# Performance work log

Hardware: AMD Instinct MI355X
Metric: run time of the kernel (lower is better)

Reference implementation:

```python
import jax, jax.numpy as jnp
import numpy as np

B, S = 8, 1024
DM = 512            # d_model arg
D = 2 * DM          # actual feature width (1024)
H = 16
DK = D // H         # 64
DV = 2 * 32         # per-head value dim (2*d_v) = 64
DI = 2048           # d_inner
K = 4               # d_conv, dilation 2 -> effective 7, pad 3 each side
EPS = 1e-6


def setup_inputs() -> dict:
    key = jax.random.key(0)
    ks = jax.random.split(key, 16)
    s = lambda k, shape, fan: jax.random.normal(k, shape, jnp.float32) / np.sqrt(fan)
    return {
        "x": jax.random.normal(ks[0], (B, S, D), jnp.float32),
        "mask": jnp.ones((B, 1, 1, S), jnp.int32),
        "gamma": jnp.ones((D,), jnp.float32),
        "wq": s(ks[1], (D, H * DK), D),
        "wk": s(ks[2], (D, H * DK), D),
        "wv": s(ks[3], (D, H * DV), D),
        "wo": s(ks[4], (H * DV, D), H * DV),
        "w1": s(ks[5], (DM, DI), DM),
        "b1": jnp.zeros((DI,), jnp.float32),
        "cw": s(ks[6], (DI, 1, K), K),   # depthwise conv kernel [O, I/groups=1, K]
        "cb": jnp.zeros((DI,), jnp.float32),
        "w2": s(ks[7], (DM, DI), DM),
        "b2": jnp.zeros((DI,), jnp.float32),
        "wp": s(ks[8], (DI, D), DI),
        "bp": jnp.zeros((D,), jnp.float32),
    }


def reference(x, mask, gamma, wq, wk, wv, wo, w1, b1, cw, cb, w2, b2, wp, bp):
    # RMSNorm
    nrm = x * jax.lax.rsqrt(jnp.mean(x * x, axis=-1, keepdims=True) + EPS) * gamma
    # Multi-head attention
    q = (nrm @ wq).reshape(B, S, H, DK).transpose(0, 2, 1, 3)
    k = (nrm @ wk).reshape(B, S, H, DK).transpose(0, 2, 1, 3)
    v = (nrm @ wv).reshape(B, S, H, DV).transpose(0, 2, 1, 3)
    scores = jnp.einsum('bhqd,bhkd->bhqk', q, k) / np.sqrt(DK).astype(np.float32)
    scores = jnp.where(mask == 0, jnp.float32(-1e9), scores)
    attn = jax.nn.softmax(scores, axis=-1)
    ctx = jnp.einsum('bhqk,bhkd->bhqd', attn, v)        # [B,H,S,DV]
    ctx = ctx.transpose(0, 2, 1, 3).reshape(B, S, H * DV)
    out = ctx @ wo                                       # [B,S,D]
    # split into two halves
    f_in, s_in = out[:, :, :D // 2], out[:, :, D // 2:]
    # FirstSection: linear -> depthwise dilated conv (padding 'same')
    f = f_in @ w1 + b1                                   # [B,S,DI]
    f = f.transpose(0, 2, 1)                             # [B,DI,S]
    f = jax.lax.conv_general_dilated(
        f, cw, window_strides=(1,), padding=[(3, 3)], rhs_dilation=(2,),
        feature_group_count=DI, dimension_numbers=('NCH', 'OIH', 'NCH'))
    f = (f + cb[None, :, None]).transpose(0, 2, 1)       # [B,S,DI]
    # SecondSection: linear + relu
    sec = jax.nn.relu(s_in @ w2 + b2)                    # [B,S,DI]
    gated = f * sec
    return x + (gated @ wp + bp)
```

## Files before the change

kernel.cpp:

```cpp
#include <hip/hip_runtime.h>

typedef unsigned short u16;
typedef __bf16 bf16x8 __attribute__((ext_vector_type(8)));
typedef short  s16x8  __attribute__((ext_vector_type(8)));
typedef float  f32x4  __attribute__((ext_vector_type(4)));

#define LDSPAD 72

#define GLOAD16(gp, lp) __builtin_amdgcn_global_load_lds( \
  (__attribute__((address_space(1))) unsigned int*)(unsigned long long)(const void*)(gp), \
  (__attribute__((address_space(3))) unsigned int*)(lp), 16, 0, 0)

static __device__ __forceinline__ u16 f2bf(float f){
  union { float f; unsigned int u; } v; v.f = f;
  unsigned int r = v.u + 0x7fffu + ((v.u >> 16) & 1u);
  return (u16)(r >> 16);
}
static __device__ __forceinline__ float bf2f(u16 u){
  union { unsigned int u; float f; } v; v.u = ((unsigned int)u) << 16; return v.f;
}
static __device__ __forceinline__ unsigned fbits(float f){
  union { float f; unsigned u; } v; v.f = f; return v.u;
}

__global__ __launch_bounds__(256) void wtrans4_kernel(
    const float* __restrict__ in0, const float* __restrict__ in1,
    const float* __restrict__ in2, const float* __restrict__ in3,
    u16* __restrict__ out0, u16* __restrict__ out1,
    u16* __restrict__ out2, u16* __restrict__ out3, int K, int N){
  __shared__ float tile[32][33];
  int z = blockIdx.z;
  const float* in = (z == 0) ? in0 : (z == 1) ? in1 : (z == 2) ? in2 : in3;
  u16* out = (z == 0) ? out0 : (z == 1) ? out1 : (z == 2) ? out2 : out3;
  int n0 = blockIdx.x * 32, k0 = blockIdx.y * 32;
  int tx = threadIdx.x, ty = threadIdx.y;
  #pragma unroll
  for (int i = 0; i < 4; ++i)
    tile[ty + i*8][tx] = in[(size_t)(k0 + ty + i*8) * N + n0 + tx];
  __syncthreads();
  #pragma unroll
  for (int i = 0; i < 4; ++i)
    out[(size_t)(n0 + ty + i*8) * K + k0 + tx] = f2bf(tile[tx][ty + i*8]);
}

__global__ __launch_bounds__(256) void cwtrans_kernel(const float* __restrict__ cw,
                                                      float* __restrict__ cwT){
  int i = blockIdx.x * 256 + threadIdx.x;
  int c = i >> 2, j = i & 3;
  cwT[j * 2048 + c] = cw[i];
}

__global__ __launch_bounds__(256) void rmsnorm_kernel(const float* __restrict__ x,
                                                      const float* __restrict__ gamma,
                                                      u16* __restrict__ out){
  int row = blockIdx.x;
  const float* xr = x + (size_t)row * 1024;
  int tid = threadIdx.x;
  float4 xv = *(const float4*)(xr + tid * 4);
  float ss = xv.x*xv.x + xv.y*xv.y + xv.z*xv.z + xv.w*xv.w;
  #pragma unroll
  for (int off = 1; off < 64; off <<= 1) ss += __shfl_xor(ss, off);
  __shared__ float wsum[4];
  if ((tid & 63) == 0) wsum[tid >> 6] = ss;
  __syncthreads();
  float tot = wsum[0] + wsum[1] + wsum[2] + wsum[3];
  float r = rsqrtf(tot * (1.0f/1024.0f) + 1e-6f);
  const float4 gv = *(const float4*)(gamma + tid * 4);
  u16* o = out + (size_t)row * 1024 + tid * 4;
  o[0] = f2bf(xv.x * r * gv.x);
  o[1] = f2bf(xv.y * r * gv.y);
  o[2] = f2bf(xv.z * r * gv.z);
  o[3] = f2bf(xv.w * r * gv.w);
}

template<int EPI>
__global__ __launch_bounds__(256) void gemm128_kernel(
    const u16* __restrict__ A, int lda,
    const u16* __restrict__ Bt,
    const float* __restrict__ bias,
    const float* __restrict__ resid,
    u16* __restrict__ outb, float* __restrict__ outf,
    u16* __restrict__ vt,
    int N, int K, float scale, int nm)
{
  __shared__ __align__(16) u16 As[2][128*64];
  __shared__ __align__(16) u16 Bs[2][128*64];
  int tid = threadIdx.x;
  int wid = tid >> 6, lane = tid & 63;
  int fr = lane & 15, fq = lane >> 4;
  int wr = wid >> 1, wc = wid & 1;
  int l = (int)blockIdx.x;
  int m0 = (l % nm) * 128, n0 = (l / nm) * 128;
  int srow = lane >> 3;
  int csw  = (lane & 7) ^ srow;
  int c7   = fr & 7;
  f32x4 acc[4][4] = {};

  const u16* Abase = A  + (size_t)m0 * lda;
  const u16* Bbase = Bt + (size_t)n0 * K;

  auto STAGE = [&](int bsel, int kt){
    int k0 = kt << 6;
    #pragma unroll
    for (int i = 0; i < 4; ++i){
      int r = i*32 + wid*8;
      GLOAD16(Abase + (size_t)(r + srow) * lda + k0 + csw*8, &As[bsel][r*64]);
      GLOAD16(Bbase + (size_t)(r + srow) * K   + k0 + csw*8, &Bs[bsel][r*64]);
    }
  };

  int nt = K >> 6;
  STAGE(0, 0);
  __syncthreads();
  for (int kt = 0; kt < nt; ++kt){
    int cur = kt & 1;
    if (kt + 1 < nt) STAGE(cur ^ 1, kt + 1);
    #pragma unroll
    for (int ks = 0; ks < 2; ++ks){
      bf16x8 av[4], bv[4];
      #pragma unroll
      for (int mi = 0; mi < 4; ++mi)
        av[mi] = *(const bf16x8*)&As[cur][(wr*64 + mi*16 + fr)*64 + (((ks*4 + fq) ^ c7) * 8)];
      #pragma unroll
      for (int ni = 0; ni < 4; ++ni)
        bv[ni] = *(const bf16x8*)&Bs[cur][(wc*64 + ni*16 + fr)*64 + (((ks*4 + fq) ^ c7) * 8)];
      #pragma unroll
      for (int mi = 0; mi < 4; ++mi)
        #pragma unroll
        for (int ni = 0; ni < 4; ++ni)
          acc[mi][ni] = __builtin_amdgcn_mfma_f32_16x16x32_bf16(av[mi], bv[ni], acc[mi][ni], 0, 0, 0);
    }
    __syncthreads();
  }

  if (EPI == 5 && n0 >= 2048){
    u16* Ct = &As[0][0];
    #pragma unroll
    for (int p = 0; p < 2; ++p){
      __syncthreads();
      if (wc == p){
        #pragma unroll
        for (int ni = 0; ni < 4; ++ni)
          #pragma unroll
          for (int mi = 0; mi < 4; ++mi){
            int cl = ni*16 + fr;
            int rl = wr*64 + mi*16 + fq*4;
            uint2 pk;
            pk.x = (unsigned)f2bf(acc[mi][ni][0]) | ((unsigned)f2bf(acc[mi][ni][1]) << 16);
            pk.y = (unsigned)f2bf(acc[mi][ni][2]) | ((unsigned)f2bf(acc[mi][ni][3]) << 16);
            *(uint2*)&Ct[cl*136 + rl] = pk;
          }
      }
      __syncthreads();
      #pragma unroll
      for (int ci = 0; ci < 4; ++ci){
        int qq = ci*256 + tid;
        int c = qq >> 4, off = (qq & 15) * 8;
        uint4 v = *(const uint4*)&Ct[c*136 + off];
        *(uint4*)&vt[(size_t)(n0 - 2048 + p*64 + c) * 8192 + m0 + off] = v;
      }
    }
    return;
  }

  #pragma unroll
  for (int ni = 0; ni < 4; ++ni){
    int col = n0 + wc*64 + ni*16 + fr;
    float bvv = (EPI >= 1 && EPI <= 3) ? bias[col] : 0.0f;
    float scl = (EPI == 5) ? ((col < 1024) ? scale : 1.0f) : scale;
    #pragma unroll
    for (int mi = 0; mi < 4; ++mi){
      #pragma unroll
      for (int j = 0; j < 4; ++j){
        int row = m0 + wr*64 + mi*16 + fq*4 + j;
        float vv = acc[mi][ni][j] * scl + bvv;
        if (EPI == 2) vv = fmaxf(vv, 0.0f);
        size_t idx = (size_t)row * N + col;
        if (EPI == 3) outf[idx] = vv + resid[idx];
        else          outb[idx] = f2bf(vv);
      }
    }
  }
}

__global__ __launch_bounds__(256) void attn_kernel(
    const u16* __restrict__ qkv, const u16* __restrict__ Vt,
    const int* __restrict__ mask, u16* __restrict__ ctx)
{
  __shared__ __align__(16) u16 Ks[64*64];
  __shared__ __align__(16) u16 Vs[64*64];
  __shared__ __align__(16) u16 Ps[64][LDSPAD];
  int tid = threadIdx.x;
  int wid = tid >> 6, lane = tid & 63;
  int fr = lane & 15, fq = lane >> 4;
  int i = (int)blockIdx.x;
  int wg = (i & 7) * 256 + (i >> 3);
  int bh = wg >> 4;
  int q0 = (wg & 15) * 64;
  int b = bh >> 4, h = bh & 15;

  const u16* qb  = qkv + (size_t)b * 1024 * 3072 + h * 64;
  const u16* kb  = qb + 1024;
  const u16* vtb = Vt + (size_t)(h * 64) * 8192 + b * 1024;

  int lrow = lane >> 3;
  int cs   = (lane & 7) ^ lrow;
  int wbase = wid * 16;
  int c7 = fr & 7;

  bf16x8 qf[2];
  {
    const u16* qp = qb + (size_t)(q0 + wid*16 + fr) * 3072 + fq * 8;
    qf[0] = *(const bf16x8*)(qp);
    qf[1] = *(const bf16x8*)(qp + 32);
  }
  f32x4 acc[4];
  #pragma unroll
  for (int k = 0; k < 4; ++k) acc[k] = (f32x4){0.f, 0.f, 0.f, 0.f};
  float mrun = -1e30f, lsum = 0.f;

  auto STAGE = [&](int t){
    int kv0 = t * 64;
    #pragma unroll
    for (int k = 0; k < 2; ++k){
      int r = wbase + k*8 + lrow;
      GLOAD16(kb  + (size_t)(kv0 + r) * 3072 + cs * 8, &Ks[(wbase + k*8) * 64]);
      GLOAD16(vtb + (size_t)r * 8192 + kv0 + cs * 8,   &Vs[(wbase + k*8) * 64]);
    }
  };

  STAGE(0);
  for (int t = 0; t < 16; ++t){
    int kv0 = t * 64;
    __syncthreads();
    bf16x8 kf[2][4], vf[2][4];
    #pragma unroll
    for (int ks = 0; ks < 2; ++ks)
      #pragma unroll
      for (int nt = 0; nt < 4; ++nt){
        kf[ks][nt] = *(const bf16x8*)&Ks[(nt*16 + fr)*64 + (((ks*4 + fq) ^ c7) * 8)];
        vf[ks][nt] = *(const bf16x8*)&Vs[(nt*16 + fr)*64 + (((ks*4 + fq) ^ c7) * 8)];
      }
    int mv1 = mask[b * 1024 + kv0 + lane];
    __syncthreads();
    if (t + 1 < 16) STAGE(t + 1);

    f32x4 sc[4];
    #pragma unroll
    for (int nt = 0; nt < 4; ++nt) sc[nt] = (f32x4){0.f, 0.f, 0.f, 0.f};
    __builtin_amdgcn_s_setprio(1);
    #pragma unroll
    for (int ks = 0; ks < 2; ++ks)
      #pragma unroll
      for (int nt = 0; nt < 4; ++nt)
        sc[nt] = __builtin_amdgcn_mfma_f32_16x16x32_bf16(kf[ks][nt], qf[ks], sc[nt], 0, 0, 0);
    __builtin_amdgcn_s_setprio(0);

    if (!__all(mv1 != 0)){
      #pragma unroll
      for (int nt = 0; nt < 4; ++nt){
        int4 mv = *(const int4*)&mask[b * 1024 + kv0 + nt*16 + fq*4];
        int mvals[4] = {mv.x, mv.y, mv.z, mv.w};
        #pragma unroll
        for (int j = 0; j < 4; ++j)
          sc[nt][j] = mvals[j] ? sc[nt][j] : -1e9f;
      }
    }

    float m01 = fmaxf(fmaxf(sc[0][0], sc[0][1]), fmaxf(sc[0][2], sc[0][3]));
    float m11 = fmaxf(fmaxf(sc[1][0], sc[1][1]), fmaxf(sc[1][2], sc[1][3]));
    float m21 = fmaxf(fmaxf(sc[2][0], sc[2][1]), fmaxf(sc[2][2], sc[2][3]));
    float m31 = fmaxf(fmaxf(sc[3][0], sc[3][1]), fmaxf(sc[3][2], sc[3][3]));
    float pmax = fmaxf(fmaxf(m01, m11), fmaxf(m21, m31));
    pmax = fmaxf(pmax, __shfl_xor(pmax, 16));
    pmax = fmaxf(pmax, __shfl_xor(pmax, 32));
    if (!__all(pmax <= mrun + 8.0f)){
      float mnew = fmaxf(mrun, pmax);
      float corr = exp2f(mrun - mnew);
      #pragma unroll
      for (int nt = 0; nt < 4; ++nt)
        #pragma unroll
        for (int j = 0; j < 4; ++j)
          acc[nt][j] *= corr;
      lsum *= corr;
      mrun = mnew;
    }
    float p[4][4];
    float ls = 0.f;
    #pragma unroll
    for (int nt = 0; nt < 4; ++nt)
      #pragma unroll
      for (int j = 0; j < 4; ++j){
        float pv = exp2f(sc[nt][j] - mrun);
        p[nt][j] = pv;
        ls += pv;
      }
    lsum += ls;

    #pragma unroll
    for (int nt = 0; nt < 4; ++nt){
      unsigned d0 = __builtin_amdgcn_perm(fbits(p[nt][1]), fbits(p[nt][0]), 0x07060302u);
      unsigned d1 = __builtin_amdgcn_perm(fbits(p[nt][3]), fbits(p[nt][2]), 0x07060302u);
      *(unsigned*)&Ps[wid*16 + fr][nt*16 + fq*4]     = d0;
      *(unsigned*)&Ps[wid*16 + fr][nt*16 + fq*4 + 2] = d1;
    }

    __builtin_amdgcn_s_setprio(1);
    #pragma unroll
    for (int ks = 0; ks < 2; ++ks){
      bf16x8 pb = *(const bf16x8*)&Ps[wid*16 + fr][ks*32 + fq*8];
      #pragma unroll
      for (int nt = 0; nt < 4; ++nt)
        acc[nt] = __builtin_amdgcn_mfma_f32_16x16x32_bf16(vf[ks][nt], pb, acc[nt], 0, 0, 0);
    }
    __builtin_amdgcn_s_setprio(0);
  }

  lsum += __shfl_xor(lsum, 16);
  lsum += __shfl_xor(lsum, 32);
  float invl = 1.0f / lsum;

  size_t rowbase = ((size_t)b * 1024 + q0 + wid*16 + fr) * 1024 + h * 64;
  #pragma unroll
  for (int nt = 0; nt < 4; ++nt){
    unsigned lo = (unsigned)f2bf(acc[nt][0] * invl) | ((unsigned)f2bf(acc[nt][1] * invl) << 16);
    unsigned hi = (unsigned)f2bf(acc[nt][2] * invl) | ((unsigned)f2bf(acc[nt][3] * invl) << 16);
    uint2 pk; pk.x = lo; pk.y = hi;
    *(uint2*)&ctx[rowbase + nt*16 + fq*4] = pk;
  }
}

__global__ __launch_bounds__(256) void convgate_kernel(
    const u16* __restrict__ f, const float* __restrict__ cwT,
    const float* __restrict__ cb, u16* __restrict__ sec_inout)
{
  size_t gid = (size_t)blockIdx.x * blockDim.x + threadIdx.x;
  int c0 = (int)(gid & 255) * 8;
  int t  = (int)((gid >> 8) & 1023);
  int b  = (int)(gid >> 18);
  const u16* fb = f + ((size_t)b * 1024) * 2048;

  float4 w[4][2];
  #pragma unroll
  for (int j = 0; j < 4; ++j){
    w[j][0] = *(const float4*)&cwT[j*2048 + c0];
    w[j][1] = *(const float4*)&cwT[j*2048 + c0 + 4];
  }
  float4 cb0 = *(const float4*)&cb[c0];
  float4 cb1 = *(const float4*)&cb[c0 + 4];
  float acc[8] = {cb0.x, cb0.y, cb0.z, cb0.w, cb1.x, cb1.y, cb1.z, cb1.w};

  #pragma unroll
  for (int j = 0; j < 4; ++j){
    int tt = t - 3 + 2 * j;
    if (tt >= 0 && tt < 1024){
      s16x8 fv = *(const s16x8*)(fb + (size_t)tt * 2048 + c0);
      const float* wj = (const float*)&w[j][0];
      #pragma unroll
      for (int e = 0; e < 8; ++e) acc[e] += bf2f((u16)fv[e]) * wj[e];
    }
  }
  u16* sp = sec_inout + (((size_t)b * 1024 + t) * 2048 + c0);
  s16x8 sv = *(const s16x8*)sp;
  s16x8 ov;
  #pragma unroll
  for (int e = 0; e < 8; ++e) ov[e] = (short)f2bf(acc[e] * bf2f((u16)sv[e]));
  *(s16x8*)sp = ov;
}

extern "C" void kernel_launch(void* const* d_in, const int* in_sizes, int n_in,
                              void* d_out, int out_size, void* d_ws, size_t ws_size,
                              hipStream_t stream)
{
  const float* x     = (const float*)d_in[0];
  const int*   mask  = (const int*)  d_in[1];
  const float* gamma = (const float*)d_in[2];
  const float* wq    = (const float*)d_in[3];
  const float* wk    = (const float*)d_in[4];
  const float* wv    = (const float*)d_in[5];
  const float* wo    = (const float*)d_in[6];
  const float* w1    = (const float*)d_in[7];
  const float* b1    = (const float*)d_in[8];
  const float* cw    = (const float*)d_in[9];
  const float* cb    = (const float*)d_in[10];
  const float* w2    = (const float*)d_in[11];
  const float* b2    = (const float*)d_in[12];
  const float* wp    = (const float*)d_in[13];
  const float* bp    = (const float*)d_in[14];
  float* out = (float*)d_out;

  char* p = (char*)d_ws;
  auto alloc = [&](size_t bytes){ char* r = p; p += (bytes + 255) & ~(size_t)255; return r; };
  u16*   wqkvT = (u16*)alloc((size_t)3072*1024*2);
  u16*   woT   = (u16*)alloc((size_t)1024*1024*2);
  u16*   w1T   = (u16*)alloc((size_t)2048*512*2);
  u16*   w2T   = (u16*)alloc((size_t)2048*512*2);
  u16*   wpT   = (u16*)alloc((size_t)1024*2048*2);
  float* cwT   = (float*)alloc((size_t)4*2048*4);
  u16*   nrm   = (u16*)alloc((size_t)8192*1024*2);
  u16*   qkv   = (u16*)alloc((size_t)8192*3072*2);
  u16*   sec   = (u16*)alloc((size_t)8192*2048*2);
  u16* Vt   = sec;
  u16* ao   = qkv;
  u16* fbuf = qkv + (size_t)8192*1024;
  (void)ws_size; (void)in_sizes; (void)n_in; (void)out_size;

  const float QSCALE = 0.125f * 1.44269504088896340736f;

  dim3 tb32(32, 8);
  wtrans4_kernel<<<dim3(32, 32, 4), tb32, 0, stream>>>(
      wq, wk, wv, wo,
      wqkvT, wqkvT + (size_t)1024*1024, wqkvT + (size_t)2048*1024, woT, 1024, 1024);
  wtrans4_kernel<<<dim3(64, 16, 2), tb32, 0, stream>>>(
      w1, w2, w1, w2, w1T, w2T, w1T, w2T, 512, 2048);
  wtrans4_kernel<<<dim3(32, 64, 1), tb32, 0, stream>>>(
      wp, wp, wp, wp, wpT, wpT, wpT, wpT, 2048, 1024);
  cwtrans_kernel<<<32, 256, 0, stream>>>(cw, cwT);

  rmsnorm_kernel<<<8192, 256, 0, stream>>>(x, gamma, nrm);

  gemm128_kernel<5><<<1536, 256, 0, stream>>>(nrm, 1024, wqkvT, nullptr, nullptr, qkv, nullptr, Vt, 3072, 1024, QSCALE, 64);

  attn_kernel<<<2048, 256, 0, stream>>>(qkv, Vt, mask, nrm);

  gemm128_kernel<0><<<512, 256, 0, stream>>>(nrm, 1024, woT, nullptr, nullptr, ao, nullptr, nullptr, 1024, 1024, 1.0f, 64);

  gemm128_kernel<1><<<1024, 256, 0, stream>>>(ao,       1024, w1T, b1, nullptr, fbuf, nullptr, nullptr, 2048, 512, 1.0f, 64);
  gemm128_kernel<2><<<1024, 256, 0, stream>>>(ao + 512, 1024, w2T, b2, nullptr, sec,  nullptr, nullptr, 2048, 512, 1.0f, 64);

  convgate_kernel<<<8192, 256, 0, stream>>>(fbuf, cwT, cb, sec);

  gemm128_kernel<3><<<512, 256, 0, stream>>>(sec, 2048, wpT, bp, x, nullptr, out, nullptr, 1024, 2048, 1.0f, 64);
}
```

Baseline: 311.9 us.

## Load K/V fragments directly from global memory in attention, dropping LDS staging

The attention kernel no longer stages K and V tiles into shared memory with async global-to-LDS copies and barriers. Each wave instead reads its MFMA operand fragments for K and V straight from global memory inside the loop. This removes two block-wide syncs per tile and the LDS round trip. In exchange, the four waves in a block each fetch the same K/V data through the cache, and there is no prefetch overlap, so load latency sits directly before the matrix ops.

```diff
diff --git a/kernel.cpp b/kernel.cpp
--- a/kernel.cpp
+++ b/kernel.cpp
@@ -187,8 +187,6 @@
     const u16* __restrict__ qkv, const u16* __restrict__ Vt,
     const int* __restrict__ mask, u16* __restrict__ ctx)
 {
-  __shared__ __align__(16) u16 Ks[64*64];
-  __shared__ __align__(16) u16 Vs[64*64];
   __shared__ __align__(16) u16 Ps[64][LDSPAD];
   int tid = threadIdx.x;
   int wid = tid >> 6, lane = tid & 63;
@@ -203,10 +201,8 @@
   const u16* kb  = qb + 1024;
   const u16* vtb = Vt + (size_t)(h * 64) * 8192 + b * 1024;
 
-  int lrow = lane >> 3;
-  int cs   = (lane & 7) ^ lrow;
-  int wbase = wid * 16;
-  int c7 = fr & 7;
+  const u16* kR = kb  + (size_t)fr * 3072 + fq * 8;
+  const u16* vR = vtb + (size_t)fr * 8192 + fq * 8;
 
   bf16x8 qf[2];
   {
@@ -219,41 +215,21 @@
   for (int k = 0; k < 4; ++k) acc[k] = (f32x4){0.f, 0.f, 0.f, 0.f};
   float mrun = -1e30f, lsum = 0.f;
 
-  auto STAGE = [&](int t){
-    int kv0 = t * 64;
-    #pragma unroll
-    for (int k = 0; k < 2; ++k){
-      int r = wbase + k*8 + lrow;
-      GLOAD16(kb  + (size_t)(kv0 + r) * 3072 + cs * 8, &Ks[(wbase + k*8) * 64]);
-      GLOAD16(vtb + (size_t)r * 8192 + kv0 + cs * 8,   &Vs[(wbase + k*8) * 64]);
-    }
-  };
-
-  STAGE(0);
   for (int t = 0; t < 16; ++t){
     int kv0 = t * 64;
-    __syncthreads();
-    bf16x8 kf[2][4], vf[2][4];
+
+    f32x4 sc[4];
+    #pragma unroll
+    for (int nt = 0; nt < 4; ++nt) sc[nt] = (f32x4){0.f, 0.f, 0.f, 0.f};
+    int mv1 = mask[b * 1024 + kv0 + lane];
+    __builtin_amdgcn_s_setprio(1);
     #pragma unroll
     for (int ks = 0; ks < 2; ++ks)
       #pragma unroll
       for (int nt = 0; nt < 4; ++nt){
-        kf[ks][nt] = *(const bf16x8*)&Ks[(nt*16 + fr)*64 + (((ks*4 + fq) ^ c7) * 8)];
-        vf[ks][nt] = *(const bf16x8*)&Vs[(nt*16 + fr)*64 + (((ks*4 + fq) ^ c7) * 8)];
-      }
-    int mv1 = mask[b * 1024 + kv0 + lane];
-    __syncthreads();
-    if (t + 1 < 16) STAGE(t + 1);
-
-    f32x4 sc[4];
-    #pragma unroll
-    for (int nt = 0; nt < 4; ++nt) sc[nt] = (f32x4){0.f, 0.f, 0.f, 0.f};
-    __builtin_amdgcn_s_setprio(1);
-    #pragma unroll
-    for (int ks = 0; ks < 2; ++ks)
-      #pragma unroll
-      for (int nt = 0; nt < 4; ++nt)
-        sc[nt] = __builtin_amdgcn_mfma_f32_16x16x32_bf16(kf[ks][nt], qf[ks], sc[nt], 0, 0, 0);
+        bf16x8 kf = *(const bf16x8*)(kR + (size_t)(kv0 + nt*16) * 3072 + ks*32);
+        sc[nt] = __builtin_amdgcn_mfma_f32_16x16x32_bf16(kf, qf[ks], sc[nt], 0, 0, 0);
+      }
     __builtin_amdgcn_s_setprio(0);
 
     if (!__all(mv1 != 0)){
@@ -285,22 +261,21 @@
       lsum *= corr;
       mrun = mnew;
     }
-    float p[4][4];
     float ls = 0.f;
     #pragma unroll
     for (int nt = 0; nt < 4; ++nt)
       #pragma unroll
       for (int j = 0; j < 4; ++j){
         float pv = exp2f(sc[nt][j] - mrun);
-        p[nt][j] = pv;
+        sc[nt][j] = pv;
         ls += pv;
       }
     lsum += ls;
 
     #pragma unroll
     for (int nt = 0; nt < 4; ++nt){
-      unsigned d0 = __builtin_amdgcn_perm(fbits(p[nt][1]), fbits(p[nt][0]), 0x07060302u);
-      unsigned d1 = __builtin_amdgcn_perm(fbits(p[nt][3]), fbits(p[nt][2]), 0x07060302u);
+      unsigned d0 = __builtin_amdgcn_perm(fbits(sc[nt][1]), fbits(sc[nt][0]), 0x07060302u);
+      unsigned d1 = __builtin_amdgcn_perm(fbits(sc[nt][3]), fbits(sc[nt][2]), 0x07060302u);
       *(unsigned*)&Ps[wid*16 + fr][nt*16 + fq*4]     = d0;
       *(unsigned*)&Ps[wid*16 + fr][nt*16 + fq*4 + 2] = d1;
     }
@@ -310,8 +285,10 @@
     for (int ks = 0; ks < 2; ++ks){
       bf16x8 pb = *(const bf16x8*)&Ps[wid*16 + fr][ks*32 + fq*8];
       #pragma unroll
-      for (int nt = 0; nt < 4; ++nt)
-        acc[nt] = __builtin_amdgcn_mfma_f32_16x16x32_bf16(vf[ks][nt], pb, acc[nt], 0, 0, 0);
+      for (int nt = 0; nt < 4; ++nt){
+        bf16x8 vv = *(const bf16x8*)(vR + (size_t)(nt*16) * 8192 + kv0 + ks*32);
+        acc[nt] = __builtin_amdgcn_mfma_f32_16x16x32_bf16(vv, pb, acc[nt], 0, 0, 0);
+      }
     }
     __builtin_amdgcn_s_setprio(0);
   }
```

Result: slower. 460.4 us (+47.6%).

## Single-buffer GEMM LDS for occupancy and merge w1/w2 GEMMs into one launch

Applied to the files above, without the earlier changes.

The GEMM kernel drops its double-buffered LDS staging for a single 32KB buffer, so each k-step loads, synchronizes and then computes. This halves LDS use per block, which may let more blocks run per CU, but load latency is no longer hidden behind compute. The two FirstSection and SecondSection GEMMs are also merged into one launch with a new epilogue that chooses bias, ReLU and output buffer by column, using a concatenated transposed weight. This saves one kernel launch and its tail.

```diff
diff --git a/kernel.cpp b/kernel.cpp
--- a/kernel.cpp
+++ b/kernel.cpp
@@ -78,13 +78,14 @@
     const u16* __restrict__ A, int lda,
     const u16* __restrict__ Bt,
     const float* __restrict__ bias,
-    const float* __restrict__ resid,
+    const float* __restrict__ b2x,
     u16* __restrict__ outb, float* __restrict__ outf,
     u16* __restrict__ vt,
     int N, int K, float scale, int nm)
 {
-  __shared__ __align__(16) u16 As[2][128*64];
-  __shared__ __align__(16) u16 Bs[2][128*64];
+  __shared__ __align__(16) u16 Sh[2*128*64];
+  u16* As = Sh;
+  u16* Bs = Sh + 128*64;
   int tid = threadIdx.x;
   int wid = tid >> 6, lane = tid & 63;
   int fr = lane & 15, fq = lane >> 4;
@@ -96,45 +97,43 @@
   int c7   = fr & 7;
   f32x4 acc[4][4] = {};
 
-  const u16* Abase = A  + (size_t)m0 * lda;
+  const u16* Abase = A + ((EPI == 6 && n0 >= 2048) ? 512 : 0) + (size_t)m0 * lda;
   const u16* Bbase = Bt + (size_t)n0 * K;
 
-  auto STAGE = [&](int bsel, int kt){
+  auto STAGE = [&](int kt){
     int k0 = kt << 6;
     #pragma unroll
     for (int i = 0; i < 4; ++i){
       int r = i*32 + wid*8;
-      GLOAD16(Abase + (size_t)(r + srow) * lda + k0 + csw*8, &As[bsel][r*64]);
-      GLOAD16(Bbase + (size_t)(r + srow) * K   + k0 + csw*8, &Bs[bsel][r*64]);
+      GLOAD16(Abase + (size_t)(r + srow) * lda + k0 + csw*8, &As[r*64]);
+      GLOAD16(Bbase + (size_t)(r + srow) * K   + k0 + csw*8, &Bs[r*64]);
     }
   };
 
   int nt = K >> 6;
-  STAGE(0, 0);
-  __syncthreads();
   for (int kt = 0; kt < nt; ++kt){
-    int cur = kt & 1;
-    if (kt + 1 < nt) STAGE(cur ^ 1, kt + 1);
+    if (kt) __syncthreads();
+    STAGE(kt);
+    __syncthreads();
     #pragma unroll
     for (int ks = 0; ks < 2; ++ks){
       bf16x8 av[4], bv[4];
       #pragma unroll
       for (int mi = 0; mi < 4; ++mi)
-        av[mi] = *(const bf16x8*)&As[cur][(wr*64 + mi*16 + fr)*64 + (((ks*4 + fq) ^ c7) * 8)];
+        av[mi] = *(const bf16x8*)&As[(wr*64 + mi*16 + fr)*64 + (((ks*4 + fq) ^ c7) * 8)];
       #pragma unroll
       for (int ni = 0; ni < 4; ++ni)
-        bv[ni] = *(const bf16x8*)&Bs[cur][(wc*64 + ni*16 + fr)*64 + (((ks*4 + fq) ^ c7) * 8)];
+        bv[ni] = *(const bf16x8*)&Bs[(wc*64 + ni*16 + fr)*64 + (((ks*4 + fq) ^ c7) * 8)];
       #pragma unroll
       for (int mi = 0; mi < 4; ++mi)
         #pragma unroll
         for (int ni = 0; ni < 4; ++ni)
           acc[mi][ni] = __builtin_amdgcn_mfma_f32_16x16x32_bf16(av[mi], bv[ni], acc[mi][ni], 0, 0, 0);
     }
-    __syncthreads();
   }
 
   if (EPI == 5 && n0 >= 2048){
-    u16* Ct = &As[0][0];
+    u16* Ct = Sh;
     #pragma unroll
     for (int p = 0; p < 2; ++p){
       __syncthreads();
@@ -166,7 +165,11 @@
   #pragma unroll
   for (int ni = 0; ni < 4; ++ni){
     int col = n0 + wc*64 + ni*16 + fr;
-    float bvv = (EPI >= 1 && EPI <= 3) ? bias[col] : 0.0f;
+    bool fp = (EPI != 6) || (col < 2048);
+    int cc  = (EPI == 6) ? (col & 2047) : col;
+    float bvv = 0.0f;
+    if (EPI == 3) bvv = bias[col];
+    if (EPI == 6) bvv = fp ? bias[cc] : b2x[cc];
     float scl = (EPI == 5) ? ((col < 1024) ? scale : 1.0f) : scale;
     #pragma unroll
     for (int mi = 0; mi < 4; ++mi){
@@ -174,10 +177,12 @@
       for (int j = 0; j < 4; ++j){
         int row = m0 + wr*64 + mi*16 + fq*4 + j;
         float vv = acc[mi][ni][j] * scl + bvv;
-        if (EPI == 2) vv = fmaxf(vv, 0.0f);
-        size_t idx = (size_t)row * N + col;
-        if (EPI == 3) outf[idx] = vv + resid[idx];
-        else          outb[idx] = f2bf(vv);
+        size_t idx = (size_t)row * N + cc;
+        if (EPI == 3)      outf[idx] = vv + b2x[idx];
+        else if (EPI == 6){
+          if (!fp) vv = fmaxf(vv, 0.0f);
+          (fp ? outb : vt)[idx] = f2bf(vv);
+        } else             outb[idx] = f2bf(vv);
       }
     }
   }
@@ -393,8 +398,7 @@
   auto alloc = [&](size_t bytes){ char* r = p; p += (bytes + 255) & ~(size_t)255; return r; };
   u16*   wqkvT = (u16*)alloc((size_t)3072*1024*2);
   u16*   woT   = (u16*)alloc((size_t)1024*1024*2);
-  u16*   w1T   = (u16*)alloc((size_t)2048*512*2);
-  u16*   w2T   = (u16*)alloc((size_t)2048*512*2);
+  u16*   w12T  = (u16*)alloc((size_t)4096*512*2);
   u16*   wpT   = (u16*)alloc((size_t)1024*2048*2);
   float* cwT   = (float*)alloc((size_t)4*2048*4);
   u16*   nrm   = (u16*)alloc((size_t)8192*1024*2);
@@ -412,7 +416,7 @@
       wq, wk, wv, wo,
       wqkvT, wqkvT + (size_t)1024*1024, wqkvT + (size_t)2048*1024, woT, 1024, 1024);
   wtrans4_kernel<<<dim3(64, 16, 2), tb32, 0, stream>>>(
-      w1, w2, w1, w2, w1T, w2T, w1T, w2T, 512, 2048);
+      w1, w2, w1, w2, w12T, w12T + (size_t)2048*512, w12T, w12T + (size_t)2048*512, 512, 2048);
   wtrans4_kernel<<<dim3(32, 64, 1), tb32, 0, stream>>>(
       wp, wp, wp, wp, wpT, wpT, wpT, wpT, 2048, 1024);
   cwtrans_kernel<<<32, 256, 0, stream>>>(cw, cwT);
@@ -425,8 +429,7 @@
 
   gemm128_kernel<0><<<512, 256, 0, stream>>>(nrm, 1024, woT, nullptr, nullptr, ao, nullptr, nullptr, 1024, 1024, 1.0f, 64);
 
-  gemm128_kernel<1><<<1024, 256, 0, stream>>>(ao,       1024, w1T, b1, nullptr, fbuf, nullptr, nullptr, 2048, 512, 1.0f, 64);
-  gemm128_kernel<2><<<1024, 256, 0, stream>>>(ao + 512, 1024, w2T, b2, nullptr, sec,  nullptr, nullptr, 2048, 512, 1.0f, 64);
+  gemm128_kernel<6><<<2048, 256, 0, stream>>>(ao, 1024, w12T, b1, b2, fbuf, nullptr, sec, 2048, 512, 1.0f, 64);
 
   convgate_kernel<<<8192, 256, 0, stream>>>(fbuf, cwT, cb, sec);
 
```

Result: no change. 312.3 us (+0.1%).
